# Performance work log

Measured on AMD Instinct MI355X. Metric: run time of the kernel, lower is better.

The kernel has to match this reference:

```python
import jax, jax.numpy as jnp
import numpy as np

N = 100_000   # nodes
E = 1_600_000 # edges
G = 128       # graphs in batch
DIN, DOUT = 100, 200


def setup_inputs() -> dict:
    key = jax.random.key(0)
    ks = jax.random.split(key, 12)
    def lin_w(k, fan_in, fan_out):
        return (jax.random.normal(k, (fan_in, fan_out), jnp.float32) / np.sqrt(fan_in)).astype(jnp.float32)
    return {
        "x": jax.random.normal(ks[0], (N, DIN), jnp.float32),
        "edge_index": jax.random.randint(ks[1], (2, E), 0, N, dtype=jnp.int32),
        "batch": jnp.sort(jax.random.randint(ks[2], (N,), 0, G, dtype=jnp.int32)),
        "W1": lin_w(ks[3], DIN, DOUT),  "b1": jnp.zeros((DOUT,), jnp.float32),
        "Wc": lin_w(ks[4], DOUT, DOUT), "bc": jnp.zeros((DOUT,), jnp.float32),
        "W2": lin_w(ks[5], DOUT, DOUT), "b2": jnp.zeros((DOUT,), jnp.float32),
        "W3": lin_w(ks[6], DOUT, DOUT), "b3": jnp.zeros((DOUT,), jnp.float32),
        "Wcls": lin_w(ks[7], DOUT, 2),  "bcls": jnp.zeros((2,), jnp.float32),
    }


def gcn_conv(x, W, b, src, dst, n_nodes):
    """PyG GCNConv: D^{-1/2}(A+I)D^{-1/2} X W + b, symmetric norm with self-loops."""
    h = x @ W  # [N, Dout]
    # degree at targets including the self-loop (+1)
    deg = jax.ops.segment_sum(jnp.ones((src.shape[0],), x.dtype), dst, num_segments=n_nodes) + 1.0
    dinv = jax.lax.rsqrt(deg)  # [N]
    # gather -> normalize -> scatter-add (messages along edges)
    msg = h[src] * (dinv[src] * dinv[dst])[:, None]          # [E, Dout]
    agg = jax.ops.segment_sum(msg, dst, num_segments=n_nodes)  # [N, Dout]
    # self-loop contribution handled analytically: norm_ii = dinv[i]^2
    agg = agg + h * (dinv * dinv)[:, None]
    return agg + b


def reference(x, edge_index, batch, W1, b1, Wc, bc, W2, b2, W3, b3, Wcls, bcls):
    src, dst = edge_index[0], edge_index[1]
    h = jax.nn.relu(gcn_conv(x, W1, b1, src, dst, N))
    # dropout is identity at eval time
    h = h @ Wc + bc
    h = jax.nn.relu(gcn_conv(h, W2, b2, src, dst, N))
    h = gcn_conv(h, W3, b3, src, dst, N)
    pooled = jax.ops.segment_max(h, batch, num_segments=G)  # global max pool -> [G, Dout]
    logits = pooled @ Wcls + bcls
    return jax.nn.softmax(logits, axis=1)
```

## Files before the change

kernel.cpp:

```cpp
#include <hip/hip_runtime.h>
#include <stdint.h>

#define N_NODES 100000
#define N_EDGES 1600000
#define N_GRAPHS 128
#define DIN 100
#define DOUT 200
#define LDH 200
#define LDX 128
#define LDT 248

#define NB 391
#define BCAP 5120
#define EPB 2048
#define NBLK 782

typedef unsigned short u16;
typedef unsigned int u32;
typedef _Float16 f16;
typedef f16 half8 __attribute__((ext_vector_type(8)));
typedef f16 half4 __attribute__((ext_vector_type(4)));
typedef f16 half2v __attribute__((ext_vector_type(2)));
typedef float floatx4 __attribute__((ext_vector_type(4)));

__device__ __forceinline__ float h2f(u16 h) {
  f16 x; __builtin_memcpy(&x, &h, 2); return (float)x;
}
__device__ __forceinline__ u16 f2h(float f) {
  f16 x = (f16)f; u16 r; __builtin_memcpy(&r, &x, 2); return r;
}
__device__ __forceinline__ u32 encmax(float f) {
  u32 b; __builtin_memcpy(&b, &f, 4);
  return (b & 0x80000000u) ? ~b : (b | 0x80000000u);
}

__device__ __forceinline__ void pack_frag(const float* __restrict__ W, int K, int nfrag,
                                          u16* __restrict__ out, int idx) {
  if (idx >= nfrag) return;
  int lane = idx & 63;
  int t = idx >> 6;
  int ct = t % 13, ks = t / 13;
  int n = ct * 16 + (lane & 15);
  int kbase = ks * 32 + (lane >> 4) * 8;
  u16 v[8];
  #pragma unroll
  for (int j = 0; j < 8; ++j) {
    int k = kbase + j;
    float f = (k < K && n < DOUT) ? W[(size_t)k * DOUT + n] : 0.f;
    v[j] = f2h(f);
  }
  uint4 o;
  o.x = (u32)v[0] | ((u32)v[1] << 16);
  o.y = (u32)v[2] | ((u32)v[3] << 16);
  o.z = (u32)v[4] | ((u32)v[5] << 16);
  o.w = (u32)v[6] | ((u32)v[7] << 16);
  *(uint4*)(out + (size_t)idx * 8) = o;
}

#define B_GB    391
#define B_COMB  549
#define B_PK1   562
#define B_PK3   585
#define B_TOT   (585 + NBLK)
__global__ void k_prep(const int* __restrict__ batch, int* __restrict__ gstart,
                       int* __restrict__ gend, const int* __restrict__ dst,
                       int* __restrict__ histAll,
                       const float* __restrict__ Wc, const float* __restrict__ bc,
                       const float* __restrict__ W2, float* __restrict__ Wc2,
                       float* __restrict__ bc2, const float* __restrict__ W1,
                       const float* __restrict__ W3, u16* __restrict__ Wpk1,
                       u16* __restrict__ Wpk3) {
  int b = blockIdx.x, t = threadIdx.x;
  if (b < B_GB) {
    int i = b * 256 + t;
    if (i >= N_NODES) return;
    int g = batch[i];
    if (i == 0 || batch[i - 1] != g) gstart[g] = i;
    if (i == N_NODES - 1 || batch[i + 1] != g) gend[g] = i;
  } else if (b < B_COMB) {
    int gid = (b - B_GB) * 256 + t;
    if (gid >= 201 * DOUT) return;
    int r = gid / DOUT, c = gid % DOUT;
    const float* a = (r < DOUT) ? (Wc + (size_t)r * DOUT) : bc;
    float s = 0.f;
    for (int k = 0; k < DOUT; ++k) s += a[k] * W2[(size_t)k * DOUT + c];
    if (r < DOUT) Wc2[(size_t)r * DOUT + c] = s;
    else bc2[c] = s;
  } else if (b < B_PK1) {
    pack_frag(W1, DIN, 4 * 13 * 64, Wpk1, (b - B_COMB) * 256 + t);
  } else if (b < B_PK3) {
    pack_frag(W3, DOUT, 7 * 13 * 64, Wpk3, (b - B_PK1) * 256 + t);
  } else {
    __shared__ int hist[NB];
    int hb = b - B_PK3;
    int e0 = hb * EPB;
    int e1 = min(e0 + EPB, N_EDGES);
    for (int j = t; j < NB; j += 256) hist[j] = 0;
    __syncthreads();
    for (int i = e0 + t; i < e1; i += 256)
      atomicAdd(&hist[dst[i] >> 8], 1);
    __syncthreads();
    for (int j = t; j < NB; j += 256)
      histAll[(size_t)hb * NB + j] = hist[j];
  }
}

#define SCAN_TOT (NB + 23)
__global__ void k_scan(const int* __restrict__ histAll, int* __restrict__ baseAll,
                       int* __restrict__ gcur, const float* __restrict__ Wc2,
                       u16* __restrict__ Wpk2) {
  int j = blockIdx.x, t = threadIdx.x;
  if (j >= NB) {
    pack_frag(Wc2, DOUT, 7 * 13 * 64, Wpk2, (j - NB) * 256 + t);
    return;
  }
  __shared__ int s[256];
  int run = 0;
  for (int c = 0; c < NBLK; c += 256) {
    int idx = c + t;
    int v = (idx < NBLK) ? histAll[(size_t)idx * NB + j] : 0;
    s[t] = v;
    __syncthreads();
    for (int o = 1; o < 256; o <<= 1) {
      int x = (t >= o) ? s[t - o] : 0;
      __syncthreads();
      s[t] += x;
      __syncthreads();
    }
    if (idx < NBLK) baseAll[(size_t)idx * NB + j] = run + s[t] - v;
    run += s[255];
    __syncthreads();
  }
  if (t == 0) gcur[j] = run;
}

__global__ void k_scatter(const int* __restrict__ src, const int* __restrict__ dst,
                          const int* __restrict__ baseAll, uint2* __restrict__ ebuf) {
  __shared__ int cur[NB];
  int b = blockIdx.x, t = threadIdx.x;
  int e0 = b * EPB;
  int e1 = min(e0 + EPB, N_EDGES);
  for (int j = t; j < NB; j += 256) cur[j] = baseAll[(size_t)b * NB + j];
  __syncthreads();
  for (int i = e0 + t; i < e1; i += 256) {
    int d = dst[i];
    int bk = d >> 8;
    int pos = atomicAdd(&cur[bk], 1);
    if (pos < BCAP)
      ebuf[(size_t)bk * BCAP + pos] = make_uint2((u32)d, (u32)src[i]);
  }
}

__global__ void k_csr(const uint2* __restrict__ ebuf, const int* __restrict__ gcur,
                      int* __restrict__ rowptr, float* __restrict__ dinv,
                      int* __restrict__ colv, const float* __restrict__ x,
                      u16* __restrict__ xs) {
  __shared__ int s_cnt[256];
  __shared__ int s_cur[256];
  __shared__ int s_scan[256];
  __shared__ int s_g[NB];
  __shared__ int s_red[256];
  __shared__ float s_dinv[256];
  int b = blockIdx.x, t = threadIdx.x;
  for (int j = t; j < NB; j += 256) s_g[j] = gcur[j];
  s_cnt[t] = 0;
  __syncthreads();
  int pacc = 0;
  for (int i = t; i < b; i += 256) pacc += s_g[i];
  s_red[t] = pacc;
  __syncthreads();
  for (int o = 128; o > 0; o >>= 1) {
    if (t < o) s_red[t] += s_red[t + o];
    __syncthreads();
  }
  int base = s_red[0];
  if (b == NB - 1 && t == 0) rowptr[N_NODES] = base + s_g[b];
  int cnt = s_g[b];
  int node0 = b << 8;
  const uint2* eb = ebuf + (size_t)b * BCAP;
  for (int i = t; i < cnt; i += 256)
    atomicAdd(&s_cnt[eb[i].x & 255], 1);
  __syncthreads();
  int v = s_cnt[t];
  s_scan[t] = v;
  __syncthreads();
  for (int o = 1; o < 256; o <<= 1) {
    int x2 = (t >= o) ? s_scan[t - o] : 0;
    __syncthreads();
    s_scan[t] += x2;
    __syncthreads();
  }
  int run = s_scan[t] - v;
  s_cur[t] = base + run;
  float dval = rsqrtf((float)v + 1.0f);
  s_dinv[t] = dval;
  int node = node0 + t;
  if (node < N_NODES) {
    rowptr[node] = base + run;
    dinv[node] = dval;
  }
  __syncthreads();
  for (int i = t; i < cnt; i += 256) {
    uint2 e = eb[i];
    int pos = atomicAdd(&s_cur[e.x & 255], 1);
    colv[pos] = (int)e.y;
  }
  for (int idx = t; idx < 256 * 50; idx += 256) {
    int nl = idx / 50, c = idx % 50;
    int nd = node0 + nl;
    if (nd < N_NODES) {
      float d = s_dinv[nl];
      float2 vv = *(const float2*)(x + (size_t)nd * DIN + c * 2);
      half2v o; o[0] = (f16)(d * vv.x); o[1] = (f16)(d * vv.y);
      *(half2v*)(xs + (size_t)nd * LDX + c * 2) = o;
    }
  }
}

__global__ __launch_bounds__(256) void k_gemm12(const u16* __restrict__ A,
                                                const u16* __restrict__ Wpk1,
                                                const float* __restrict__ b1,
                                                const u16* __restrict__ Wpk2,
                                                const float* __restrict__ bc2,
                                                const float* __restrict__ dinv,
                                                u16* __restrict__ C, int nrows) {
  __shared__ u16 tile[4][32][LDT];
  int wv = threadIdx.x >> 6;
  int lane = threadIdx.x & 63;
  int r0 = blockIdx.x * 128 + wv * 32;
  int m = lane & 15, q = lane >> 4;
  int row0 = r0 + m, row1 = r0 + 16 + m;
  bool ok0 = (row0 < nrows), ok1 = (row1 < nrows);

  floatx4 acc0[13], acc1[13];
  #pragma unroll
  for (int ct = 0; ct < 13; ++ct) {
    acc0[ct] = floatx4{0.f, 0.f, 0.f, 0.f};
    acc1[ct] = floatx4{0.f, 0.f, 0.f, 0.f};
  }

  {
    const u16* a0p = A + (size_t)row0 * LDX + q * 8;
    const u16* a1p = A + (size_t)row1 * LDX + q * 8;
    const u16* wp = Wpk1 + (size_t)lane * 8;
    #pragma unroll
    for (int ks = 0; ks < 4; ++ks) {
      half8 a0 = ok0 ? *(const half8*)(a0p + ks * 32) : half8{0, 0, 0, 0, 0, 0, 0, 0};
      half8 a1 = ok1 ? *(const half8*)(a1p + ks * 32) : half8{0, 0, 0, 0, 0, 0, 0, 0};
      #pragma unroll
      for (int ct = 0; ct < 13; ++ct) {
        half8 bfr = *(const half8*)(wp + (size_t)(ks * 13 + ct) * 512);
        acc0[ct] = __builtin_amdgcn_mfma_f32_16x16x32_f16(a0, bfr, acc0[ct], 0, 0, 0);
        acc1[ct] = __builtin_amdgcn_mfma_f32_16x16x32_f16(a1, bfr, acc1[ct], 0, 0, 0);
      }
    }
  }

  for (int idx = lane; idx < 32 * ((LDT - 200) / 2); idx += 64) {
    int rr = idx / ((LDT - 200) / 2);
    int cc = 200 + (idx % ((LDT - 200) / 2)) * 2;
    *(half2v*)&tile[wv][rr][cc] = half2v{0, 0};
  }
  #pragma unroll
  for (int ct = 0; ct < 13; ++ct) {
    int c = ct * 16 + m;
    if (c >= DOUT) continue;
    float bv = b1[c];
    #pragma unroll
    for (int rg = 0; rg < 4; ++rg) {
      tile[wv][q * 4 + rg][c]      = f2h(fmaxf(acc0[ct][rg] + bv, 0.f));
      tile[wv][16 + q * 4 + rg][c] = f2h(fmaxf(acc1[ct][rg] + bv, 0.f));
    }
  }
  __syncthreads();

  #pragma unroll
  for (int ct = 0; ct < 13; ++ct) {
    acc0[ct] = floatx4{0.f, 0.f, 0.f, 0.f};
    acc1[ct] = floatx4{0.f, 0.f, 0.f, 0.f};
  }
  {
    const u16* wp = Wpk2 + (size_t)lane * 8;
    #pragma unroll
    for (int ks = 0; ks < 7; ++ks) {
      half8 a0 = *(const half8*)&tile[wv][m][q * 8 + ks * 32];
      half8 a1 = *(const half8*)&tile[wv][16 + m][q * 8 + ks * 32];
      #pragma unroll
      for (int ct = 0; ct < 13; ++ct) {
        half8 bfr = *(const half8*)(wp + (size_t)(ks * 13 + ct) * 512);
        acc0[ct] = __builtin_amdgcn_mfma_f32_16x16x32_f16(a0, bfr, acc0[ct], 0, 0, 0);
        acc1[ct] = __builtin_amdgcn_mfma_f32_16x16x32_f16(a1, bfr, acc1[ct], 0, 0, 0);
      }
    }
  }

  float sc0[4], sc1[4];
  #pragma unroll
  for (int rg = 0; rg < 4; ++rg) {
    int or0 = r0 + q * 4 + rg;
    int or1 = r0 + 16 + q * 4 + rg;
    sc0[rg] = (or0 < nrows) ? dinv[or0] : 1.f;
    sc1[rg] = (or1 < nrows) ? dinv[or1] : 1.f;
  }
  #pragma unroll
  for (int ct = 0; ct < 13; ++ct) {
    int c = ct * 16 + m;
    if (c >= DOUT) continue;
    float bv = bc2[c];
    #pragma unroll
    for (int rg = 0; rg < 4; ++rg) {
      int or0 = r0 + q * 4 + rg;
      if (or0 < nrows)
        C[(size_t)or0 * LDH + c] = f2h((acc0[ct][rg] + bv) * sc0[rg]);
      int or1 = r0 + 16 + q * 4 + rg;
      if (or1 < nrows)
        C[(size_t)or1 * LDH + c] = f2h((acc1[ct][rg] + bv) * sc1[rg]);
    }
  }
}

template <int NKS>
__global__ __launch_bounds__(256) void k_gemm_mfma(const u16* __restrict__ A, int lda,
                                                   const u16* __restrict__ Wpk,
                                                   const float* __restrict__ bias,
                                                   const float* __restrict__ rowscale,
                                                   u16* __restrict__ C, int relu, int nrows) {
  int wv = threadIdx.x >> 6;
  int lane = threadIdx.x & 63;
  int r0 = blockIdx.x * 128 + wv * 32;
  int m = lane & 15, q = lane >> 4;
  int row0 = r0 + m, row1 = r0 + 16 + m;
  bool ok0 = (row0 < nrows), ok1 = (row1 < nrows);
  const u16* a0p = A + (size_t)row0 * lda + q * 8;
  const u16* a1p = A + (size_t)row1 * lda + q * 8;

  floatx4 acc0[13], acc1[13];
  #pragma unroll
  for (int ct = 0; ct < 13; ++ct) {
    acc0[ct] = floatx4{0.f, 0.f, 0.f, 0.f};
    acc1[ct] = floatx4{0.f, 0.f, 0.f, 0.f};
  }

  const u16* wp = Wpk + (size_t)lane * 8;
  #pragma unroll
  for (int ks = 0; ks < NKS; ++ks) {
    half8 a0 = ok0 ? *(const half8*)(a0p + ks * 32) : half8{0, 0, 0, 0, 0, 0, 0, 0};
    half8 a1 = ok1 ? *(const half8*)(a1p + ks * 32) : half8{0, 0, 0, 0, 0, 0, 0, 0};
    #pragma unroll
    for (int ct = 0; ct < 13; ++ct) {
      half8 bfr = *(const half8*)(wp + (size_t)(ks * 13 + ct) * 512);
      acc0[ct] = __builtin_amdgcn_mfma_f32_16x16x32_f16(a0, bfr, acc0[ct], 0, 0, 0);
      acc1[ct] = __builtin_amdgcn_mfma_f32_16x16x32_f16(a1, bfr, acc1[ct], 0, 0, 0);
    }
  }

  float sc0[4], sc1[4];
  #pragma unroll
  for (int rg = 0; rg < 4; ++rg) {
    int or0 = r0 + q * 4 + rg;
    int or1 = r0 + 16 + q * 4 + rg;
    sc0[rg] = (rowscale && or0 < nrows) ? rowscale[or0] : 1.f;
    sc1[rg] = (rowscale && or1 < nrows) ? rowscale[or1] : 1.f;
  }

  #pragma unroll
  for (int ct = 0; ct < 13; ++ct) {
    int c = ct * 16 + m;
    if (c >= DOUT) continue;
    float bv = bias ? bias[c] : 0.f;
    #pragma unroll
    for (int rg = 0; rg < 4; ++rg) {
      int or0 = r0 + q * 4 + rg;
      if (or0 < nrows) {
        float v = acc0[ct][rg] + bv;
        if (relu) v = fmaxf(v, 0.f);
        C[(size_t)or0 * LDH + c] = f2h(v * sc0[rg]);
      }
      int or1 = r0 + 16 + q * 4 + rg;
      if (or1 < nrows) {
        float v = acc1[ct][rg] + bv;
        if (relu) v = fmaxf(v, 0.f);
        C[(size_t)or1 * LDH + c] = f2h(v * sc1[rg]);
      }
    }
  }
}

__global__ void k_agg200h(const u16* __restrict__ T, const float* __restrict__ dinv,
                          const int* __restrict__ rowptr, const int* __restrict__ col,
                          const float* __restrict__ bias, u16* __restrict__ OUT,
                          int relu) {
  int wave = (blockIdx.x * blockDim.x + threadIdx.x) >> 6;
  int lane = threadIdx.x & 63;
  if (wave >= N_NODES || lane >= 50) return;
  int node = wave;
  int c4 = lane * 4;
  int beg = __builtin_amdgcn_readfirstlane(rowptr[node]);
  int end = __builtin_amdgcn_readfirstlane(rowptr[node + 1]);
  half4 sv = *(const half4*)(T + (size_t)node * LDH + c4);
  float di = dinv[node];
  float ax = 0.f, ay = 0.f, az = 0.f, aw = 0.f;
  int e = beg;
  for (; e + 16 <= end; e += 16) {
    int s[16];
    half4 tv[16];
    #pragma unroll
    for (int j = 0; j < 16; ++j) s[j] = col[e + j];
    #pragma unroll
    for (int j = 0; j < 16; ++j)
      tv[j] = *(const half4*)(T + (size_t)s[j] * LDH + c4);
    #pragma unroll
    for (int j = 0; j < 16; ++j) {
      ax += (float)tv[j][0]; ay += (float)tv[j][1];
      az += (float)tv[j][2]; aw += (float)tv[j][3];
    }
  }
  if (e + 8 <= end) {
    int s[8];
    half4 tv[8];
    #pragma unroll
    for (int j = 0; j < 8; ++j) s[j] = col[e + j];
    #pragma unroll
    for (int j = 0; j < 8; ++j)
      tv[j] = *(const half4*)(T + (size_t)s[j] * LDH + c4);
    #pragma unroll
    for (int j = 0; j < 8; ++j) {
      ax += (float)tv[j][0]; ay += (float)tv[j][1];
      az += (float)tv[j][2]; aw += (float)tv[j][3];
    }
    e += 8;
  }
  if (e + 4 <= end) {
    int s[4];
    half4 tv[4];
    #pragma unroll
    for (int j = 0; j < 4; ++j) s[j] = col[e + j];
    #pragma unroll
    for (int j = 0; j < 4; ++j)
      tv[j] = *(const half4*)(T + (size_t)s[j] * LDH + c4);
    #pragma unroll
    for (int j = 0; j < 4; ++j) {
      ax += (float)tv[j][0]; ay += (float)tv[j][1];
      az += (float)tv[j][2]; aw += (float)tv[j][3];
    }
    e += 4;
  }
  for (; e < end; ++e) {
    half4 tv = *(const half4*)(T + (size_t)col[e] * LDH + c4);
    ax += (float)tv[0]; ay += (float)tv[1];
    az += (float)tv[2]; aw += (float)tv[3];
  }
  float rx = di * (ax + (float)sv[0]);
  float ry = di * (ay + (float)sv[1]);
  float rz = di * (az + (float)sv[2]);
  float rw = di * (aw + (float)sv[3]);
  if (bias) {
    rx += bias[c4 + 0]; ry += bias[c4 + 1];
    rz += bias[c4 + 2]; rw += bias[c4 + 3];
  }
  if (relu) {
    rx = fmaxf(rx, 0.f); ry = fmaxf(ry, 0.f);
    rz = fmaxf(rz, 0.f); rw = fmaxf(rw, 0.f);
  }
  half4 o;
  o[0] = (f16)rx; o[1] = (f16)ry; o[2] = (f16)rz; o[3] = (f16)rw;
  __builtin_nontemporal_store(o, (half4*)(OUT + (size_t)node * LDH + c4));
}

__global__ void k_agg100h(const u16* __restrict__ T, const float* __restrict__ dinv,
                          const int* __restrict__ rowptr, const int* __restrict__ col,
                          u16* __restrict__ OUT) {
  int wave = (blockIdx.x * blockDim.x + threadIdx.x) >> 6;
  int lane = threadIdx.x & 63;
  if (wave >= N_NODES || lane >= 50) return;
  int node = wave;
  int c2 = lane * 2;
  int beg = __builtin_amdgcn_readfirstlane(rowptr[node]);
  int end = __builtin_amdgcn_readfirstlane(rowptr[node + 1]);
  half2v sv = *(const half2v*)(T + (size_t)node * LDX + c2);
  float di = dinv[node];
  float ax = 0.f, ay = 0.f;
  int e = beg;
  for (; e + 16 <= end; e += 16) {
    int s[16];
    half2v tv[16];
    #pragma unroll
    for (int j = 0; j < 16; ++j) s[j] = col[e + j];
    #pragma unroll
    for (int j = 0; j < 16; ++j)
      tv[j] = *(const half2v*)(T + (size_t)s[j] * LDX + c2);
    #pragma unroll
    for (int j = 0; j < 16; ++j) { ax += (float)tv[j][0]; ay += (float)tv[j][1]; }
  }
  if (e + 8 <= end) {
    int s[8];
    half2v tv[8];
    #pragma unroll
    for (int j = 0; j < 8; ++j) s[j] = col[e + j];
    #pragma unroll
    for (int j = 0; j < 8; ++j)
      tv[j] = *(const half2v*)(T + (size_t)s[j] * LDX + c2);
    #pragma unroll
    for (int j = 0; j < 8; ++j) { ax += (float)tv[j][0]; ay += (float)tv[j][1]; }
    e += 8;
  }
  if (e + 4 <= end) {
    int s[4];
    half2v tv[4];
    #pragma unroll
    for (int j = 0; j < 4; ++j) s[j] = col[e + j];
    #pragma unroll
    for (int j = 0; j < 4; ++j)
      tv[j] = *(const half2v*)(T + (size_t)s[j] * LDX + c2);
    #pragma unroll
    for (int j = 0; j < 4; ++j) { ax += (float)tv[j][0]; ay += (float)tv[j][1]; }
    e += 4;
  }
  for (; e < end; ++e) {
    half2v tv = *(const half2v*)(T + (size_t)col[e] * LDX + c2);
    ax += (float)tv[0]; ay += (float)tv[1];
  }
  half2v o;
  o[0] = (f16)(di * (ax + (float)sv[0]));
  o[1] = (f16)(di * (ay + (float)sv[1]));
  __builtin_nontemporal_store(o, (half2v*)(OUT + (size_t)node * LDX + c2));
}

__global__ void k_aggpool(const u16* __restrict__ T, const float* __restrict__ dinv,
                          const int* __restrict__ rowptr, const int* __restrict__ col,
                          const float* __restrict__ bias, const int* __restrict__ batch,
                          u32* __restrict__ partenc) {
  __shared__ u32 s_enc[4][DOUT];
  int t = threadIdx.x;
  for (int i = t; i < 4 * DOUT; i += 256) ((u32*)s_enc)[i] = 0u;
  __syncthreads();
  int wv = t >> 6, lane = t & 63;
  int nb0 = blockIdx.x * 16;
  int n0 = nb0 + wv * 4;
  int gfirst = batch[nb0];
  int rpl = rowptr[n0 + (lane < 4 ? lane : 4)];
  if (lane < 50) {
    int c4 = lane * 4;
    float b0 = bias[c4 + 0], b1v = bias[c4 + 1], b2v = bias[c4 + 2], b3v = bias[c4 + 3];
    for (int i = 0; i < 4; ++i) {
      int node = n0 + i;
      int beg = __builtin_amdgcn_readlane(rpl, i);
      int end = __builtin_amdgcn_readlane(rpl, i + 1);
      half4 sv = *(const half4*)(T + (size_t)node * LDH + c4);
      float di = dinv[node];
      float ax = 0.f, ay = 0.f, az = 0.f, aw = 0.f;
      int e = beg;
      for (; e + 16 <= end; e += 16) {
        int s[16];
        half4 tv[16];
        #pragma unroll
        for (int j = 0; j < 16; ++j) s[j] = col[e + j];
        #pragma unroll
        for (int j = 0; j < 16; ++j)
          tv[j] = *(const half4*)(T + (size_t)s[j] * LDH + c4);
        #pragma unroll
        for (int j = 0; j < 16; ++j) {
          ax += (float)tv[j][0]; ay += (float)tv[j][1];
          az += (float)tv[j][2]; aw += (float)tv[j][3];
        }
      }
      if (e + 8 <= end) {
        int s[8];
        half4 tv[8];
        #pragma unroll
        for (int j = 0; j < 8; ++j) s[j] = col[e + j];
        #pragma unroll
        for (int j = 0; j < 8; ++j)
          tv[j] = *(const half4*)(T + (size_t)s[j] * LDH + c4);
        #pragma unroll
        for (int j = 0; j < 8; ++j) {
          ax += (float)tv[j][0]; ay += (float)tv[j][1];
          az += (float)tv[j][2]; aw += (float)tv[j][3];
        }
        e += 8;
      }
      if (e + 4 <= end) {
        int s[4];
        half4 tv[4];
        #pragma unroll
        for (int j = 0; j < 4; ++j) s[j] = col[e + j];
        #pragma unroll
        for (int j = 0; j < 4; ++j)
          tv[j] = *(const half4*)(T + (size_t)s[j] * LDH + c4);
        #pragma unroll
        for (int j = 0; j < 4; ++j) {
          ax += (float)tv[j][0]; ay += (float)tv[j][1];
          az += (float)tv[j][2]; aw += (float)tv[j][3];
        }
        e += 4;
      }
      for (; e < end; ++e) {
        half4 tv = *(const half4*)(T + (size_t)col[e] * LDH + c4);
        ax += (float)tv[0]; ay += (float)tv[1];
        az += (float)tv[2]; aw += (float)tv[3];
      }
      float rx = di * (ax + (float)sv[0]) + b0;
      float ry = di * (ay + (float)sv[1]) + b1v;
      float rz = di * (az + (float)sv[2]) + b2v;
      float rw = di * (aw + (float)sv[3]) + b3v;
      u32 e0 = encmax(rx), e1 = encmax(ry), e2 = encmax(rz), e3 = encmax(rw);
      int slot = batch[node] - gfirst;
      if (slot < 4) {
        atomicMax(&s_enc[slot][c4 + 0], e0);
        atomicMax(&s_enc[slot][c4 + 1], e1);
        atomicMax(&s_enc[slot][c4 + 2], e2);
        atomicMax(&s_enc[slot][c4 + 3], e3);
      } else {
        u32* p = partenc + (size_t)batch[node] * DOUT + c4;
        atomicMax(&p[0], e0); atomicMax(&p[1], e1);
        atomicMax(&p[2], e2); atomicMax(&p[3], e3);
      }
    }
  }
  __syncthreads();
  for (int i = t; i < 4 * DOUT; i += 256) {
    u32 v = ((u32*)s_enc)[i];
    if (v) {
      int slot = i / DOUT, d = i % DOUT;
      atomicMax(&partenc[(size_t)(gfirst + slot) * DOUT + d], v);
    }
  }
}

__global__ void k_poolcls(const u32* __restrict__ partenc, const float* __restrict__ Wcls,
                          const float* __restrict__ bcls, float* __restrict__ out) {
  __shared__ float l0s[256], l1s[256];
  int g = blockIdx.x, t = threadIdx.x;
  float c0 = 0.f, c1 = 0.f;
  if (t < DOUT) {
    u32 e = partenc[(size_t)g * DOUT + t];
    float mv;
    if (e == 0u) {
      mv = -3.4e38f;
    } else {
      u32 b = (e & 0x80000000u) ? (e ^ 0x80000000u) : ~e;
      __builtin_memcpy(&mv, &b, 4);
    }
    c0 = mv * Wcls[t * 2 + 0];
    c1 = mv * Wcls[t * 2 + 1];
  }
  l0s[t] = c0; l1s[t] = c1;
  __syncthreads();
  for (int o = 128; o > 0; o >>= 1) {
    if (t < o) { l0s[t] += l0s[t + o]; l1s[t] += l1s[t + o]; }
    __syncthreads();
  }
  if (t == 0) {
    float l0 = l0s[0] + bcls[0], l1 = l1s[0] + bcls[1];
    float m = fmaxf(l0, l1);
    float e0 = expf(l0 - m), e1 = expf(l1 - m);
    float inv = 1.0f / (e0 + e1);
    out[g * 2 + 0] = e0 * inv;
    out[g * 2 + 1] = e1 * inv;
  }
}

static inline size_t align256(size_t x) { return (x + 255) & ~(size_t)255; }

extern "C" void kernel_launch(void* const* d_in, const int* in_sizes, int n_in,
                              void* d_out, int out_size, void* d_ws, size_t ws_size,
                              hipStream_t stream) {
  const float* x     = (const float*)d_in[0];
  const int*   ei    = (const int*)d_in[1];
  const int*   batch = (const int*)d_in[2];
  const float* W1    = (const float*)d_in[3];
  const float* b1    = (const float*)d_in[4];
  const float* Wc    = (const float*)d_in[5];
  const float* bc    = (const float*)d_in[6];
  const float* W2    = (const float*)d_in[7];
  const float* b2    = (const float*)d_in[8];
  const float* W3    = (const float*)d_in[9];
  const float* b3    = (const float*)d_in[10];
  const float* Wcls  = (const float*)d_in[11];
  const float* bcls  = (const float*)d_in[12];
  float* out = (float*)d_out;

  const int N = N_NODES, E = N_EDGES;
  const int* src = ei;
  const int* dst = ei + E;

  char* ws = (char*)d_ws;
  size_t off = 0;
  float* dinv    = (float*)(ws + off); off = align256(off + (size_t)N * 4);
  int*   rowptr  = (int*)  (ws + off); off = align256(off + (size_t)(N + 1) * 4);
  int*   col     = (int*)  (ws + off); off = align256(off + (size_t)E * 4);
  int*   gcur    = (int*)  (ws + off); off = align256(off + (size_t)NB * 4);
  int*   histAll = (int*)  (ws + off); off = align256(off + (size_t)NBLK * NB * 4);
  int*   baseAll = (int*)  (ws + off); off = align256(off + (size_t)NBLK * NB * 4);
  int*   gstart  = (int*)  (ws + off); off = align256(off + 512);
  int*   gend    = (int*)  (ws + off); off = align256(off + 512);
  float* Wc2     = (float*)(ws + off); off = align256(off + (size_t)DOUT * DOUT * 4);
  float* bc2     = (float*)(ws + off); off = align256(off + (size_t)DOUT * 4);
  u16*   Wpk1    = (u16*)  (ws + off); off = align256(off + (size_t)4 * 13 * 64 * 8 * 2);
  u16*   Wpk2    = (u16*)  (ws + off); off = align256(off + (size_t)7 * 13 * 64 * 8 * 2);
  u16*   Wpk3    = (u16*)  (ws + off); off = align256(off + (size_t)7 * 13 * 64 * 8 * 2);
  u16*   xs      = (u16*)  (ws + off); off = align256(off + ((size_t)N * LDX + 128) * 2);
  u16*   bufX    = (u16*)  (ws + off); off = align256(off + ((size_t)N * LDX + 128) * 2);
  u16*   buf0    = (u16*)  (ws + off); off = align256(off + ((size_t)N * LDH + 128) * 2);
  u16*   buf1    = (u16*)  (ws + off); off = align256(off + ((size_t)N * LDH + 128) * 2);
  u16*   buf2    = (u16*)  (ws + off); off = align256(off + ((size_t)N * LDH + 128) * 2);

  uint2* ebuf    = (uint2*)buf0;
  u32*   partenc = (u32*)bufX;

  k_prep<<<B_TOT, 256, 0, stream>>>(batch, gstart, gend, dst, histAll,
                                    Wc, bc, W2, Wc2, bc2, W1, W3, Wpk1, Wpk3);
  k_scan<<<SCAN_TOT, 256, 0, stream>>>(histAll, baseAll, gcur, Wc2, Wpk2);
  k_scatter<<<NBLK, 256, 0, stream>>>(src, dst, baseAll, ebuf);
  k_csr<<<NB, 256, 0, stream>>>(ebuf, gcur, rowptr, dinv, col, x, xs);

  int gemmb = (N + 127) / 128;
  int aggb  = (N + 3) / 4;
  int aggpb = N / 16;

  k_agg100h<<<aggb, 256, 0, stream>>>(xs, dinv, rowptr, col, bufX);
  k_gemm12<<<gemmb, 256, 0, stream>>>(bufX, Wpk1, b1, Wpk2, bc2, dinv, buf2, N);
  hipMemsetAsync(partenc, 0, (size_t)N_GRAPHS * DOUT * 4, stream);
  k_agg200h<<<aggb, 256, 0, stream>>>(buf2, dinv, rowptr, col, b2, buf0, 1);
  k_gemm_mfma<7><<<gemmb, 256, 0, stream>>>(buf0, LDH, Wpk3, nullptr, dinv, buf1, 0, N);
  k_aggpool<<<aggpb, 256, 0, stream>>>(buf1, dinv, rowptr, col, b3, batch, partenc);
  k_poolcls<<<N_GRAPHS, 256, 0, stream>>>(partenc, Wcls, bcls, out);
}
```

Before: 653.4 us.

## Split fused double GEMM, drop unused graph-bounds pass, fold pool memset into CSR

Replaces the fused k_gemm12 kernel, which chained both linear layers through an LDS tile, with two calls to the generic k_gemm_mfma template that go through a global fp16 buffer. Removes the gstart/gend computation from k_prep, since nothing reads it. Drops the separate hipMemsetAsync of the pooling accumulator and zeroes it inside k_csr instead, aliasing it onto the no-longer-needed histAll buffer. This saves launches and dead work, but splitting the GEMM adds a full N×200 intermediate write and read to global memory plus an extra launch.

```diff
diff --git a/kernel.cpp b/kernel.cpp
--- a/kernel.cpp
+++ b/kernel.cpp
@@ -8,7 +8,6 @@
 #define DOUT 200
 #define LDH 200
 #define LDX 128
-#define LDT 248
 
 #define NB 391
 #define BCAP 5120
@@ -57,28 +56,19 @@
   *(uint4*)(out + (size_t)idx * 8) = o;
 }
 
-#define B_GB    391
-#define B_COMB  549
-#define B_PK1   562
-#define B_PK3   585
-#define B_TOT   (585 + NBLK)
-__global__ void k_prep(const int* __restrict__ batch, int* __restrict__ gstart,
-                       int* __restrict__ gend, const int* __restrict__ dst,
-                       int* __restrict__ histAll,
+#define B_COMB  158
+#define B_PK1   171
+#define B_PK3   194
+#define B_TOT   (194 + NBLK)
+__global__ void k_prep(const int* __restrict__ dst, int* __restrict__ histAll,
                        const float* __restrict__ Wc, const float* __restrict__ bc,
                        const float* __restrict__ W2, float* __restrict__ Wc2,
                        float* __restrict__ bc2, const float* __restrict__ W1,
                        const float* __restrict__ W3, u16* __restrict__ Wpk1,
                        u16* __restrict__ Wpk3) {
   int b = blockIdx.x, t = threadIdx.x;
-  if (b < B_GB) {
-    int i = b * 256 + t;
-    if (i >= N_NODES) return;
-    int g = batch[i];
-    if (i == 0 || batch[i - 1] != g) gstart[g] = i;
-    if (i == N_NODES - 1 || batch[i + 1] != g) gend[g] = i;
-  } else if (b < B_COMB) {
-    int gid = (b - B_GB) * 256 + t;
+  if (b < B_COMB) {
+    int gid = b * 256 + t;
     if (gid >= 201 * DOUT) return;
     int r = gid / DOUT, c = gid % DOUT;
     const float* a = (r < DOUT) ? (Wc + (size_t)r * DOUT) : bc;
@@ -154,7 +144,7 @@
 __global__ void k_csr(const uint2* __restrict__ ebuf, const int* __restrict__ gcur,
                       int* __restrict__ rowptr, float* __restrict__ dinv,
                       int* __restrict__ colv, const float* __restrict__ x,
-                      u16* __restrict__ xs) {
+                      u16* __restrict__ xs, u32* __restrict__ partenc) {
   __shared__ int s_cnt[256];
   __shared__ int s_cur[256];
   __shared__ int s_scan[256];
@@ -162,6 +152,8 @@
   __shared__ int s_red[256];
   __shared__ float s_dinv[256];
   int b = blockIdx.x, t = threadIdx.x;
+  int zid = b * 256 + t;
+  if (zid < N_GRAPHS * DOUT) partenc[zid] = 0u;
   for (int j = t; j < NB; j += 256) s_g[j] = gcur[j];
   s_cnt[t] = 0;
   __syncthreads();
@@ -213,108 +205,6 @@
       float2 vv = *(const float2*)(x + (size_t)nd * DIN + c * 2);
       half2v o; o[0] = (f16)(d * vv.x); o[1] = (f16)(d * vv.y);
       *(half2v*)(xs + (size_t)nd * LDX + c * 2) = o;
-    }
-  }
-}
-
-__global__ __launch_bounds__(256) void k_gemm12(const u16* __restrict__ A,
-                                                const u16* __restrict__ Wpk1,
-                                                const float* __restrict__ b1,
-                                                const u16* __restrict__ Wpk2,
-                                                const float* __restrict__ bc2,
-                                                const float* __restrict__ dinv,
-                                                u16* __restrict__ C, int nrows) {
-  __shared__ u16 tile[4][32][LDT];
-  int wv = threadIdx.x >> 6;
-  int lane = threadIdx.x & 63;
-  int r0 = blockIdx.x * 128 + wv * 32;
-  int m = lane & 15, q = lane >> 4;
-  int row0 = r0 + m, row1 = r0 + 16 + m;
-  bool ok0 = (row0 < nrows), ok1 = (row1 < nrows);
-
-  floatx4 acc0[13], acc1[13];
-  #pragma unroll
-  for (int ct = 0; ct < 13; ++ct) {
-    acc0[ct] = floatx4{0.f, 0.f, 0.f, 0.f};
-    acc1[ct] = floatx4{0.f, 0.f, 0.f, 0.f};
-  }
-
-  {
-    const u16* a0p = A + (size_t)row0 * LDX + q * 8;
-    const u16* a1p = A + (size_t)row1 * LDX + q * 8;
-    const u16* wp = Wpk1 + (size_t)lane * 8;
-    #pragma unroll
-    for (int ks = 0; ks < 4; ++ks) {
-      half8 a0 = ok0 ? *(const half8*)(a0p + ks * 32) : half8{0, 0, 0, 0, 0, 0, 0, 0};
-      half8 a1 = ok1 ? *(const half8*)(a1p + ks * 32) : half8{0, 0, 0, 0, 0, 0, 0, 0};
-      #pragma unroll
-      for (int ct = 0; ct < 13; ++ct) {
-        half8 bfr = *(const half8*)(wp + (size_t)(ks * 13 + ct) * 512);
-        acc0[ct] = __builtin_amdgcn_mfma_f32_16x16x32_f16(a0, bfr, acc0[ct], 0, 0, 0);
-        acc1[ct] = __builtin_amdgcn_mfma_f32_16x16x32_f16(a1, bfr, acc1[ct], 0, 0, 0);
-      }
-    }
-  }
-
-  for (int idx = lane; idx < 32 * ((LDT - 200) / 2); idx += 64) {
-    int rr = idx / ((LDT - 200) / 2);
-    int cc = 200 + (idx % ((LDT - 200) / 2)) * 2;
-    *(half2v*)&tile[wv][rr][cc] = half2v{0, 0};
-  }
-  #pragma unroll
-  for (int ct = 0; ct < 13; ++ct) {
-    int c = ct * 16 + m;
-    if (c >= DOUT) continue;
-    float bv = b1[c];
-    #pragma unroll
-    for (int rg = 0; rg < 4; ++rg) {
-      tile[wv][q * 4 + rg][c]      = f2h(fmaxf(acc0[ct][rg] + bv, 0.f));
-      tile[wv][16 + q * 4 + rg][c] = f2h(fmaxf(acc1[ct][rg] + bv, 0.f));
-    }
-  }
-  __syncthreads();
-
-  #pragma unroll
-  for (int ct = 0; ct < 13; ++ct) {
-    acc0[ct] = floatx4{0.f, 0.f, 0.f, 0.f};
-    acc1[ct] = floatx4{0.f, 0.f, 0.f, 0.f};
-  }
-  {
-    const u16* wp = Wpk2 + (size_t)lane * 8;
-    #pragma unroll
-    for (int ks = 0; ks < 7; ++ks) {
-      half8 a0 = *(const half8*)&tile[wv][m][q * 8 + ks * 32];
-      half8 a1 = *(const half8*)&tile[wv][16 + m][q * 8 + ks * 32];
-      #pragma unroll
-      for (int ct = 0; ct < 13; ++ct) {
-        half8 bfr = *(const half8*)(wp + (size_t)(ks * 13 + ct) * 512);
-        acc0[ct] = __builtin_amdgcn_mfma_f32_16x16x32_f16(a0, bfr, acc0[ct], 0, 0, 0);
-        acc1[ct] = __builtin_amdgcn_mfma_f32_16x16x32_f16(a1, bfr, acc1[ct], 0, 0, 0);
-      }
-    }
-  }
-
-  float sc0[4], sc1[4];
-  #pragma unroll
-  for (int rg = 0; rg < 4; ++rg) {
-    int or0 = r0 + q * 4 + rg;
-    int or1 = r0 + 16 + q * 4 + rg;
-    sc0[rg] = (or0 < nrows) ? dinv[or0] : 1.f;
-    sc1[rg] = (or1 < nrows) ? dinv[or1] : 1.f;
-  }
-  #pragma unroll
-  for (int ct = 0; ct < 13; ++ct) {
-    int c = ct * 16 + m;
-    if (c >= DOUT) continue;
-    float bv = bc2[c];
-    #pragma unroll
-    for (int rg = 0; rg < 4; ++rg) {
-      int or0 = r0 + q * 4 + rg;
-      if (or0 < nrows)
-        C[(size_t)or0 * LDH + c] = f2h((acc0[ct][rg] + bv) * sc0[rg]);
-      int or1 = r0 + 16 + q * 4 + rg;
-      if (or1 < nrows)
-        C[(size_t)or1 * LDH + c] = f2h((acc1[ct][rg] + bv) * sc1[rg]);
     }
   }
 }
@@ -692,8 +582,6 @@
   int*   gcur    = (int*)  (ws + off); off = align256(off + (size_t)NB * 4);
   int*   histAll = (int*)  (ws + off); off = align256(off + (size_t)NBLK * NB * 4);
   int*   baseAll = (int*)  (ws + off); off = align256(off + (size_t)NBLK * NB * 4);
-  int*   gstart  = (int*)  (ws + off); off = align256(off + 512);
-  int*   gend    = (int*)  (ws + off); off = align256(off + 512);
   float* Wc2     = (float*)(ws + off); off = align256(off + (size_t)DOUT * DOUT * 4);
   float* bc2     = (float*)(ws + off); off = align256(off + (size_t)DOUT * 4);
   u16*   Wpk1    = (u16*)  (ws + off); off = align256(off + (size_t)4 * 13 * 64 * 8 * 2);
@@ -706,21 +594,21 @@
   u16*   buf2    = (u16*)  (ws + off); off = align256(off + ((size_t)N * LDH + 128) * 2);
 
   uint2* ebuf    = (uint2*)buf0;
-  u32*   partenc = (u32*)bufX;
-
-  k_prep<<<B_TOT, 256, 0, stream>>>(batch, gstart, gend, dst, histAll,
-                                    Wc, bc, W2, Wc2, bc2, W1, W3, Wpk1, Wpk3);
+  u32*   partenc = (u32*)histAll;
+
+  k_prep<<<B_TOT, 256, 0, stream>>>(dst, histAll, Wc, bc, W2, Wc2, bc2,
+                                    W1, W3, Wpk1, Wpk3);
   k_scan<<<SCAN_TOT, 256, 0, stream>>>(histAll, baseAll, gcur, Wc2, Wpk2);
   k_scatter<<<NBLK, 256, 0, stream>>>(src, dst, baseAll, ebuf);
-  k_csr<<<NB, 256, 0, stream>>>(ebuf, gcur, rowptr, dinv, col, x, xs);
+  k_csr<<<NB, 256, 0, stream>>>(ebuf, gcur, rowptr, dinv, col, x, xs, partenc);
 
   int gemmb = (N + 127) / 128;
   int aggb  = (N + 3) / 4;
   int aggpb = N / 16;
 
   k_agg100h<<<aggb, 256, 0, stream>>>(xs, dinv, rowptr, col, bufX);
-  k_gemm12<<<gemmb, 256, 0, stream>>>(bufX, Wpk1, b1, Wpk2, bc2, dinv, buf2, N);
-  hipMemsetAsync(partenc, 0, (size_t)N_GRAPHS * DOUT * 4, stream);
+  k_gemm_mfma<4><<<gemmb, 256, 0, stream>>>(bufX, LDX, Wpk1, b1, nullptr, buf0, 1, N);
+  k_gemm_mfma<7><<<gemmb, 256, 0, stream>>>(buf0, LDH, Wpk2, bc2, dinv, buf2, 0, N);
   k_agg200h<<<aggb, 256, 0, stream>>>(buf2, dinv, rowptr, col, b2, buf0, 1);
   k_gemm_mfma<7><<<gemmb, 256, 0, stream>>>(buf0, LDH, Wpk3, nullptr, dinv, buf1, 0, N);
   k_aggpool<<<aggpb, 256, 0, stream>>>(buf1, dinv, rowptr, col, b3, batch, partenc);
```

Measured after the change: 647.3 us. About the same (-0.9%).
